# Optimization experiments

Hardware: AMD Instinct MI355X
Metric: run time of the kernel (lower is better)

Reference implementation:

```python
import jax, jax.numpy as jnp
import numpy as np

jax.config.update("jax_enable_x64", True)  # I-BERT's FixedPointMul runs in double precision

# I-BERT IntSoftmax constants
COEF0 = 0.35815147
COEF1 = 0.96963238 / COEF0
COEF2 = 1.0 / COEF0
X0 = -0.6931          # -ln(2)
N_EXP = 30            # large integer n in int_exp
MAX_BIT = 32
OUTPUT_BIT = 8
ACT_BIT = 16

B, H, S = 1, 12, 2048


def sg(x):
    return jax.lax.stop_gradient(x)


def ste_round(x):
    # straight-through round (matches torch round_ste / SymmetricQuantFunction backward)
    return x + sg(jnp.round(x) - x)


def ste_floor(x):
    return x + sg(jnp.floor(x) - x)


def sym_scale(x_min, x_max, bits):
    # symmetric_linear_quantization_params: scale = clamp(max(|min|,|max|),1e-8)/(2^(b-1)-1)
    n = 2 ** (bits - 1) - 1
    s = jnp.maximum(jnp.abs(x_min), jnp.abs(x_max))
    return sg(jnp.maximum(s, 1e-8) / n)


def fixedpoint_mul(pre_act, pre_sf, z_sf, bits):
    # I-BERT fixedpoint_mul: requantize pre_act (granularity pre_sf) to scale z_sf
    # using a 31-bit mantissa frexp decomposition, computed in float64.
    n = 2 ** (bits - 1) - 1
    z_int = ste_round(pre_act.astype(jnp.float64) / pre_sf.astype(jnp.float64))
    new_scale = sg((pre_sf / z_sf).astype(jnp.float64))
    e = jnp.floor(jnp.log2(jnp.abs(new_scale))) + 1.0   # frexp exponent
    m_int = jnp.round((new_scale / 2.0 ** e) * 2.0 ** 31)  # 31-bit mantissa
    out = ste_round(z_int * m_int / 2.0 ** (31.0 - e))
    return jnp.clip(out, -n - 1, n).astype(jnp.float32)


def quant_softmax(x):
    n16 = 2 ** (ACT_BIT - 1) - 1
    # ---- outer QuantAct(16, symmetric), specified min/max = data min/max ----
    sf = sym_scale(sg(x.min()), sg(x.max()), ACT_BIT)
    x_int = jnp.clip(ste_round(x / sf), -n16 - 1, n16)
    quant_x = x_int * sf  # dequantized activation returned by QuantAct
    # ---- IntSoftmax ----
    xi = quant_x / sf
    xi = xi - xi.max(axis=-1, keepdims=True)
    # int_exp: shift-based exponential, exp(x) = 2^(-q) * exp(r), r in (-ln2, 0]
    x0_int = sg(jnp.floor(X0 / sf))               # negative integer
    xi = jnp.maximum(xi, N_EXP * x0_int)
    q = ste_floor(xi / x0_int)
    r = xi - x0_int * q
    # int_polynomial: 2nd-order poly approximation of exp on (-ln2, 0]
    b_int = sg(jnp.floor(COEF1 / sf))
    c_int = sg(jnp.floor(COEF2 / sf ** 2))
    z = r * (r + b_int) + c_int
    exp_sf = sg(COEF0 * sf ** 2) / 2.0 ** N_EXP
    exp_int = jnp.maximum(ste_floor(z * 2.0 ** (N_EXP - q)), 0.0)
    # ---- inner QuantAct(16): requantize exp to 16 bits to avoid overflow ----
    act_sf = sym_scale(sg(exp_int.min()), sg(exp_int.max()), ACT_BIT)
    exp_int16 = fixedpoint_mul(exp_int, exp_sf, act_sf, ACT_BIT)
    # ---- integer normalization to output_bit fixed point ----
    s = exp_int16.sum(axis=-1, keepdims=True)
    factor = ste_floor(2.0 ** MAX_BIT / s)
    out_int = ste_floor(exp_int16 * factor / 2.0 ** (MAX_BIT - OUTPUT_BIT))
    out_sf = 1.0 / 2.0 ** OUTPUT_BIT
    return out_int * out_sf  # softmax probs quantized to 1/256 grid


def setup_inputs() -> dict:
    key = jax.random.key(0)
    x = jax.random.normal(key, (B, H, S, S), dtype=jnp.float32)
    return {"x": x}


def reference(x):
    return quant_softmax(x)
```

## Files before the change

### kernel.cpp

```cpp
#include <hip/hip_runtime.h>
#include <math.h>


#define ROW_S 2048
#define RPB 8
#define P1_BLOCKS (24576 / RPB)

typedef float floatx4 __attribute__((ext_vector_type(4)));

struct Scalars {
    double exp_sf_d;
    double inv_exp_sf;
    double m_int;
    double inv_pow;
    float  sf;
    float  inv_sf;
    float  x0_int;
    float  inv_x0;
    float  b_int;
    float  c_int;
    float  thirty_x0;
    float  _pad;
};

__device__ __forceinline__ float div_rn(float a, float b, float inv) {
    const float q0 = __fmul_rn(a, inv);
    const float r  = __fmaf_rn(-b, q0, a);
    return __fmaf_rn(r, inv, q0);
}
__device__ __forceinline__ double ddiv_rn(double a, double b, double inv) {
    const double q0 = __dmul_rn(a, inv);
    const double r  = __fma_rn(-b, q0, a);
    return __fma_rn(r, inv, q0);
}

__global__ __launch_bounds__(256) void k_rowmax(const float* __restrict__ x,
                                                float* __restrict__ pabs,
                                                float* __restrict__ rowmax) {
    const int t   = threadIdx.x;
    const int rib = t >> 5;
    const int lir = t & 31;
    const size_t base4 = ((size_t)blockIdx.x * RPB + rib) * (ROW_S / 4) + lir;
    const float4* x4 = (const float4*)x;

    float vmax = -INFINITY, amax = 0.0f;
#pragma unroll
    for (int k = 0; k < 16; ++k) {
        float4 v = x4[base4 + (size_t)k * 32];
        vmax = fmaxf(vmax, fmaxf(fmaxf(v.x, v.y), fmaxf(v.z, v.w)));
        amax = fmaxf(amax, fmaxf(fmaxf(fabsf(v.x), fabsf(v.y)),
                                 fmaxf(fabsf(v.z), fabsf(v.w))));
    }
#pragma unroll
    for (int m = 16; m > 0; m >>= 1) vmax = fmaxf(vmax, __shfl_xor(vmax, m));
    if (lir == 0) rowmax[blockIdx.x * RPB + rib] = vmax;
#pragma unroll
    for (int m = 32; m > 0; m >>= 1) amax = fmaxf(amax, __shfl_xor(amax, m));
    __shared__ float sa[4];
    if ((t & 63) == 0) sa[t >> 6] = amax;
    __syncthreads();
    if (t == 0) pabs[blockIdx.x] = fmaxf(fmaxf(sa[0], sa[1]), fmaxf(sa[2], sa[3]));
}

__global__ __launch_bounds__(256) void k_scalars(const float* __restrict__ pabs,
                                                 Scalars* __restrict__ sc) {
    const int tid = threadIdx.x;
    float amax = 0.0f;
    for (int i = tid; i < P1_BLOCKS; i += 256) amax = fmaxf(amax, pabs[i]);
#pragma unroll
    for (int m = 32; m > 0; m >>= 1) amax = fmaxf(amax, __shfl_xor(amax, m));
    __shared__ float sa[4];
    const int wave = tid >> 6, lane = tid & 63;
    if (lane == 0) sa[wave] = amax;
    __syncthreads();
    if (tid == 0) {
        const float sabs = fmaxf(fmaxf(sa[0], sa[1]), fmaxf(sa[2], sa[3]));
        const float sf    = __fdiv_rn(fmaxf(sabs, 1e-8f), 32767.0f);
        const float x0i   = floorf(__fdiv_rn((float)(-0.6931), sf));
        const float sfsq  = __fmul_rn(sf, sf);
        const float b_int = floorf(__fdiv_rn((float)(0.96963238 / 0.35815147), sf));
        const float c_int = floorf(__fdiv_rn((float)(1.0 / 0.35815147), sfsq));
        const float exp_sf = __fdiv_rn(__fmul_rn((float)(0.35815147), sfsq), 1073741824.0f);
        const float emax   = __fmul_rn(c_int, 1073741824.0f);
        const float act_sf = __fdiv_rn(fmaxf(emax, 1e-8f), 32767.0f);
        const float  nsf = __fdiv_rn(exp_sf, act_sf);
        const double ns  = (double)nsf;
        int E;
        (void)frexp(ns, &E);
        const double m_int = rint(ldexp(ns, 31 - E));
        sc->exp_sf_d   = (double)exp_sf;
        sc->inv_exp_sf = 1.0 / (double)exp_sf;
        sc->m_int      = m_int;
        sc->inv_pow    = ldexp(1.0, E - 31);
        sc->sf         = sf;
        sc->inv_sf     = __fdiv_rn(1.0f, sf);
        sc->x0_int     = x0i;
        sc->inv_x0     = __fdiv_rn(1.0f, x0i);
        sc->b_int      = b_int;
        sc->c_int      = c_int;
        sc->thirty_x0  = __fmul_rn(30.0f, x0i);
    }
}

__global__ __launch_bounds__(256) void k_row(const float* __restrict__ x,
                                             float* __restrict__ out,
                                             const Scalars* __restrict__ scp,
                                             const float* __restrict__ rowmax) {
    const int tid = threadIdx.x;
    const size_t rowbase = (size_t)blockIdx.x * ROW_S;
    const float4* x4 = (const float4*)(x + rowbase);
    floatx4* o4 = (floatx4*)(out + rowbase);

    const float4 va = x4[tid];
    const float4 vb = x4[tid + 256];
    const float  rm = rowmax[blockIdx.x];

    const Scalars sc = *scp;
    const float sf = sc.sf, inv_sf = sc.inv_sf;

    float ximax;
    {
        float t = rintf(div_rn(rm, sf, inv_sf));
        t = fminf(fmaxf(t, -32768.0f), 32767.0f);
        t = __fmul_rn(t, sf);
        ximax = div_rn(t, sf, inv_sf);
    }

    float xv[8] = {va.x, va.y, va.z, va.w, vb.x, vb.y, vb.z, vb.w};

    float e16[8];
    float ssum = 0.0f;
#pragma unroll
    for (int j = 0; j < 8; ++j) {
        float t = rintf(div_rn(xv[j], sf, inv_sf));
        t = fminf(fmaxf(t, -32768.0f), 32767.0f);
        t = __fmul_rn(t, sf);
        t = div_rn(t, sf, inv_sf);
        const float xs = __fsub_rn(t, ximax);
        const float xm = fmaxf(xs, sc.thirty_x0);
        const float qf = floorf(div_rn(xm, sc.x0_int, sc.inv_x0));
        const float r  = __fsub_rn(xm, __fmul_rn(sc.x0_int, qf));
        const float z  = __fadd_rn(__fmul_rn(r, __fadd_rn(r, sc.b_int)), sc.c_int);
        const int   qi = (int)qf;
        const float p2 = __int_as_float((157 - qi) << 23);
        const float ei = fmaxf(floorf(__fmul_rn(z, p2)), 0.0f);
        const double a  = (double)ei;
        const double zi = rint(ddiv_rn(a, sc.exp_sf_d, sc.inv_exp_sf));
        double ov = rint(__dmul_rn(__dmul_rn(zi, sc.m_int), sc.inv_pow));
        ov = fmin(fmax(ov, -32768.0), 32767.0);
        const float v = (float)ov;
        e16[j] = v;
        ssum += v;
    }

    __shared__ float red[4];
    const int wave = tid >> 6, lane = tid & 63;
#pragma unroll
    for (int m = 32; m > 0; m >>= 1) ssum += __shfl_xor(ssum, m);
    if (lane == 0) red[wave] = ssum;
    __syncthreads();
    const float s = ((red[0] + red[1]) + (red[2] + red[3]));
    const float factor = floorf(__fdiv_rn(4294967296.0f, s));

    float ov[8];
#pragma unroll
    for (int j = 0; j < 8; ++j) {
        const float oi = floorf(__fmul_rn(__fmul_rn(e16[j], factor), 5.9604644775390625e-8f));
        ov[j] = __fmul_rn(oi, 0.00390625f);
    }
    floatx4 w0 = {ov[0], ov[1], ov[2], ov[3]};
    floatx4 w1 = {ov[4], ov[5], ov[6], ov[7]};
    __builtin_nontemporal_store(w0, &o4[tid]);
    __builtin_nontemporal_store(w1, &o4[tid + 256]);
}

extern "C" void kernel_launch(void* const* d_in, const int* in_sizes, int n_in,
                              void* d_out, int out_size, void* d_ws, size_t ws_size,
                              hipStream_t stream) {
    const float* x = (const float*)d_in[0];
    float* out = (float*)d_out;
    const int n = in_sizes[0];
    const int rows = n / ROW_S;

    Scalars* sc   = (Scalars*)d_ws;
    float* pabs   = (float*)((char*)d_ws + 256);
    float* rowmax = (float*)((char*)d_ws + 32768);

    k_rowmax<<<P1_BLOCKS, 256, 0, stream>>>(x, pabs, rowmax);
    k_scalars<<<1, 256, 0, stream>>>(pabs, sc);
    k_row<<<rows, 256, 0, stream>>>(x, out, sc, rowmax);
}
```

Baseline: 360.7 us.

## Fuse three kernels into one persistent kernel with a grid-wide barrier

The three launches (row max, scalar computation, row softmax) become a single persistent kernel of 512 blocks. Each block handles 48 rows and meets the others at a global atomic barrier: block 0 computes the shared scalars and releases a flag. The second pass walks the rows in reverse so the most recently read data is likely still in cache (L2/MALL), cutting DRAM re-reads of the input and removing launch gaps. The cost is a spin-wait barrier that can deadlock unless all 512 blocks are co-resident. It also adds a memset of the sync counters, and row max and absolute max now use min/max tracking.

```diff
diff --git a/kernel.cpp b/kernel.cpp
--- a/kernel.cpp
+++ b/kernel.cpp
@@ -3,24 +3,21 @@
 
 
 #define ROW_S 2048
-#define RPB 8
-#define P1_BLOCKS (24576 / RPB)
+#define GRID  512
+#define TPB   256
 
 typedef float floatx4 __attribute__((ext_vector_type(4)));
 
-struct Scalars {
+struct Gsync {
+    unsigned count;
+    unsigned flag;
+    unsigned amax_bits;
+    unsigned _pad;
     double exp_sf_d;
     double inv_exp_sf;
     double m_int;
     double inv_pow;
-    float  sf;
-    float  inv_sf;
-    float  x0_int;
-    float  inv_x0;
-    float  b_int;
-    float  c_int;
-    float  thirty_x0;
-    float  _pad;
+    float  sf, inv_sf, x0_int, inv_x0, b_int, c_int, thirty_x0, _pad2;
 };
 
 __device__ __forceinline__ float div_rn(float a, float b, float inv) {
@@ -34,144 +31,148 @@
     return __fma_rn(r, inv, q0);
 }
 
-__global__ __launch_bounds__(256) void k_rowmax(const float* __restrict__ x,
-                                                float* __restrict__ pabs,
-                                                float* __restrict__ rowmax) {
-    const int t   = threadIdx.x;
-    const int rib = t >> 5;
-    const int lir = t & 31;
-    const size_t base4 = ((size_t)blockIdx.x * RPB + rib) * (ROW_S / 4) + lir;
+__global__ __launch_bounds__(TPB, 2) void k_fused(const float* __restrict__ x,
+                                                  float* __restrict__ out,
+                                                  Gsync* __restrict__ g,
+                                                  int rows) {
+    const int tid  = threadIdx.x;
+    const int wave = tid >> 6, lane = tid & 63;
+    const int rpb   = rows / GRID;
+    const int iters = rpb >> 2;
+    const int row0  = blockIdx.x * rpb;
+
+    __shared__ float rowmax_s[64];
+    __shared__ float amax_s[4];
+
     const float4* x4 = (const float4*)x;
 
-    float vmax = -INFINITY, amax = 0.0f;
+    float vminall = INFINITY, rmall = -INFINITY;
+    for (int k = 0; k < iters; ++k) {
+        const int rl = (k << 2) + wave;
+        const size_t b4 = (size_t)(row0 + rl) * (ROW_S / 4) + lane;
+        float4 v[8];
 #pragma unroll
-    for (int k = 0; k < 16; ++k) {
-        float4 v = x4[base4 + (size_t)k * 32];
-        vmax = fmaxf(vmax, fmaxf(fmaxf(v.x, v.y), fmaxf(v.z, v.w)));
-        amax = fmaxf(amax, fmaxf(fmaxf(fabsf(v.x), fabsf(v.y)),
-                                 fmaxf(fabsf(v.z), fabsf(v.w))));
+        for (int j = 0; j < 8; ++j) v[j] = x4[b4 + 64 * j];
+        float vmax = -INFINITY;
+#pragma unroll
+        for (int j = 0; j < 8; ++j) {
+            vmax    = fmaxf(vmax,    fmaxf(fmaxf(v[j].x, v[j].y), fmaxf(v[j].z, v[j].w)));
+            vminall = fminf(vminall, fminf(fminf(v[j].x, v[j].y), fminf(v[j].z, v[j].w)));
+        }
+#pragma unroll
+        for (int m = 32; m > 0; m >>= 1) vmax = fmaxf(vmax, __shfl_xor(vmax, m));
+        if (lane == 0) rowmax_s[rl] = vmax;
+        rmall = fmaxf(rmall, vmax);
     }
 #pragma unroll
-    for (int m = 16; m > 0; m >>= 1) vmax = fmaxf(vmax, __shfl_xor(vmax, m));
-    if (lir == 0) rowmax[blockIdx.x * RPB + rib] = vmax;
+    for (int m = 32; m > 0; m >>= 1) vminall = fminf(vminall, __shfl_xor(vminall, m));
+    const float am = fmaxf(-vminall, rmall);
+    if (lane == 0) amax_s[wave] = am;
+    __syncthreads();
+
+    if (tid == 0) {
+        const float amax = fmaxf(fmaxf(amax_s[0], amax_s[1]), fmaxf(amax_s[2], amax_s[3]));
+        atomicMax(&g->amax_bits, __float_as_uint(amax));
+        __threadfence();
+        atomicAdd(&g->count, 1u);
+        if (blockIdx.x == 0) {
+            while (__hip_atomic_load(&g->count, __ATOMIC_ACQUIRE, __HIP_MEMORY_SCOPE_AGENT) < GRID) {}
+            const float sabs = __uint_as_float(
+                __hip_atomic_load(&g->amax_bits, __ATOMIC_ACQUIRE, __HIP_MEMORY_SCOPE_AGENT));
+            const float sf    = __fdiv_rn(fmaxf(sabs, 1e-8f), 32767.0f);
+            const float x0i   = floorf(__fdiv_rn((float)(-0.6931), sf));
+            const float sfsq  = __fmul_rn(sf, sf);
+            const float b_int = floorf(__fdiv_rn((float)(0.96963238 / 0.35815147), sf));
+            const float c_int = floorf(__fdiv_rn((float)(1.0 / 0.35815147), sfsq));
+            const float exp_sf = __fdiv_rn(__fmul_rn((float)(0.35815147), sfsq), 1073741824.0f);
+            const float emax   = __fmul_rn(c_int, 1073741824.0f);
+            const float act_sf = __fdiv_rn(fmaxf(emax, 1e-8f), 32767.0f);
+            const float  nsf = __fdiv_rn(exp_sf, act_sf);
+            const double ns  = (double)nsf;
+            int E;
+            (void)frexp(ns, &E);
+            g->exp_sf_d   = (double)exp_sf;
+            g->inv_exp_sf = 1.0 / (double)exp_sf;
+            g->m_int      = rint(ldexp(ns, 31 - E));
+            g->inv_pow    = ldexp(1.0, E - 31);
+            g->sf         = sf;
+            g->inv_sf     = __fdiv_rn(1.0f, sf);
+            g->x0_int     = x0i;
+            g->inv_x0     = __fdiv_rn(1.0f, x0i);
+            g->b_int      = b_int;
+            g->c_int      = c_int;
+            g->thirty_x0  = __fmul_rn(30.0f, x0i);
+            __threadfence();
+            __hip_atomic_store(&g->flag, 1u, __ATOMIC_RELEASE, __HIP_MEMORY_SCOPE_AGENT);
+        }
+    }
+    while (__hip_atomic_load(&g->flag, __ATOMIC_ACQUIRE, __HIP_MEMORY_SCOPE_AGENT) == 0u) {}
+    __syncthreads();
+
+    const float  sf     = g->sf,      inv_sf = g->inv_sf;
+    const float  x0i    = g->x0_int,  inv_x0 = g->inv_x0;
+    const float  b_int  = g->b_int,   c_int  = g->c_int, t30 = g->thirty_x0;
+    const double esf    = g->exp_sf_d, iesf  = g->inv_exp_sf;
+    const double mi     = g->m_int,    ipow  = g->inv_pow;
+    (void)c_int;
+
+    floatx4* o4 = (floatx4*)out;
+    for (int k = iters - 1; k >= 0; --k) {
+        const int rl = (k << 2) + wave;
+        const size_t b4 = (size_t)(row0 + rl) * (ROW_S / 4) + lane;
+        const float rm = rowmax_s[rl];
+        float ximax;
+        {
+            float t = rintf(div_rn(rm, sf, inv_sf));
+            t = fminf(fmaxf(t, -32768.0f), 32767.0f);
+            t = __fmul_rn(t, sf);
+            ximax = div_rn(t, sf, inv_sf);
+        }
+        float4 v[8];
 #pragma unroll
-    for (int m = 32; m > 0; m >>= 1) amax = fmaxf(amax, __shfl_xor(amax, m));
-    __shared__ float sa[4];
-    if ((t & 63) == 0) sa[t >> 6] = amax;
-    __syncthreads();
-    if (t == 0) pabs[blockIdx.x] = fmaxf(fmaxf(sa[0], sa[1]), fmaxf(sa[2], sa[3]));
-}
-
-__global__ __launch_bounds__(256) void k_scalars(const float* __restrict__ pabs,
-                                                 Scalars* __restrict__ sc) {
-    const int tid = threadIdx.x;
-    float amax = 0.0f;
-    for (int i = tid; i < P1_BLOCKS; i += 256) amax = fmaxf(amax, pabs[i]);
+        for (int j = 0; j < 8; ++j) v[j] = x4[b4 + 64 * j];
+        float e16[32];
+        float ssum = 0.0f;
 #pragma unroll
-    for (int m = 32; m > 0; m >>= 1) amax = fmaxf(amax, __shfl_xor(amax, m));
-    __shared__ float sa[4];
-    const int wave = tid >> 6, lane = tid & 63;
-    if (lane == 0) sa[wave] = amax;
-    __syncthreads();
-    if (tid == 0) {
-        const float sabs = fmaxf(fmaxf(sa[0], sa[1]), fmaxf(sa[2], sa[3]));
-        const float sf    = __fdiv_rn(fmaxf(sabs, 1e-8f), 32767.0f);
-        const float x0i   = floorf(__fdiv_rn((float)(-0.6931), sf));
-        const float sfsq  = __fmul_rn(sf, sf);
-        const float b_int = floorf(__fdiv_rn((float)(0.96963238 / 0.35815147), sf));
-        const float c_int = floorf(__fdiv_rn((float)(1.0 / 0.35815147), sfsq));
-        const float exp_sf = __fdiv_rn(__fmul_rn((float)(0.35815147), sfsq), 1073741824.0f);
-        const float emax   = __fmul_rn(c_int, 1073741824.0f);
-        const float act_sf = __fdiv_rn(fmaxf(emax, 1e-8f), 32767.0f);
-        const float  nsf = __fdiv_rn(exp_sf, act_sf);
-        const double ns  = (double)nsf;
-        int E;
-        (void)frexp(ns, &E);
-        const double m_int = rint(ldexp(ns, 31 - E));
-        sc->exp_sf_d   = (double)exp_sf;
-        sc->inv_exp_sf = 1.0 / (double)exp_sf;
-        sc->m_int      = m_int;
-        sc->inv_pow    = ldexp(1.0, E - 31);
-        sc->sf         = sf;
-        sc->inv_sf     = __fdiv_rn(1.0f, sf);
-        sc->x0_int     = x0i;
-        sc->inv_x0     = __fdiv_rn(1.0f, x0i);
-        sc->b_int      = b_int;
-        sc->c_int      = c_int;
-        sc->thirty_x0  = __fmul_rn(30.0f, x0i);
+        for (int j = 0; j < 8; ++j) {
+            const float xv[4] = {v[j].x, v[j].y, v[j].z, v[j].w};
+#pragma unroll
+            for (int c = 0; c < 4; ++c) {
+                float t = rintf(div_rn(xv[c], sf, inv_sf));
+                t = fminf(fmaxf(t, -32768.0f), 32767.0f);
+                t = __fmul_rn(t, sf);
+                t = div_rn(t, sf, inv_sf);
+                const float xs = __fsub_rn(t, ximax);
+                const float xm = fmaxf(xs, t30);
+                const float qf = floorf(div_rn(xm, x0i, inv_x0));
+                const float r  = __fsub_rn(xm, __fmul_rn(x0i, qf));
+                const float z  = __fadd_rn(__fmul_rn(r, __fadd_rn(r, b_int)), c_int);
+                const int   qi = (int)qf;
+                const float p2 = __int_as_float((157 - qi) << 23);
+                const float ei = fmaxf(floorf(__fmul_rn(z, p2)), 0.0f);
+                const double zi = rint(ddiv_rn((double)ei, esf, iesf));
+                double ov = rint(__dmul_rn(__dmul_rn(zi, mi), ipow));
+                ov = fmin(fmax(ov, -32768.0), 32767.0);
+                const float w = (float)ov;
+                e16[4 * j + c] = w;
+                ssum += w;
+            }
+        }
+#pragma unroll
+        for (int m = 32; m > 0; m >>= 1) ssum += __shfl_xor(ssum, m);
+        const float factor = floorf(__fdiv_rn(4294967296.0f, ssum));
+#pragma unroll
+        for (int j = 0; j < 8; ++j) {
+            floatx4 w;
+#pragma unroll
+            for (int c = 0; c < 4; ++c) {
+                const float oi = floorf(__fmul_rn(__fmul_rn(e16[4 * j + c], factor),
+                                                  5.9604644775390625e-8f));
+                w[c] = __fmul_rn(oi, 0.00390625f);
+            }
+            __builtin_nontemporal_store(w, &o4[b4 + 64 * j]);
+        }
     }
-}
-
-__global__ __launch_bounds__(256) void k_row(const float* __restrict__ x,
-                                             float* __restrict__ out,
-                                             const Scalars* __restrict__ scp,
-                                             const float* __restrict__ rowmax) {
-    const int tid = threadIdx.x;
-    const size_t rowbase = (size_t)blockIdx.x * ROW_S;
-    const float4* x4 = (const float4*)(x + rowbase);
-    floatx4* o4 = (floatx4*)(out + rowbase);
-
-    const float4 va = x4[tid];
-    const float4 vb = x4[tid + 256];
-    const float  rm = rowmax[blockIdx.x];
-
-    const Scalars sc = *scp;
-    const float sf = sc.sf, inv_sf = sc.inv_sf;
-
-    float ximax;
-    {
-        float t = rintf(div_rn(rm, sf, inv_sf));
-        t = fminf(fmaxf(t, -32768.0f), 32767.0f);
-        t = __fmul_rn(t, sf);
-        ximax = div_rn(t, sf, inv_sf);
-    }
-
-    float xv[8] = {va.x, va.y, va.z, va.w, vb.x, vb.y, vb.z, vb.w};
-
-    float e16[8];
-    float ssum = 0.0f;
-#pragma unroll
-    for (int j = 0; j < 8; ++j) {
-        float t = rintf(div_rn(xv[j], sf, inv_sf));
-        t = fminf(fmaxf(t, -32768.0f), 32767.0f);
-        t = __fmul_rn(t, sf);
-        t = div_rn(t, sf, inv_sf);
-        const float xs = __fsub_rn(t, ximax);
-        const float xm = fmaxf(xs, sc.thirty_x0);
-        const float qf = floorf(div_rn(xm, sc.x0_int, sc.inv_x0));
-        const float r  = __fsub_rn(xm, __fmul_rn(sc.x0_int, qf));
-        const float z  = __fadd_rn(__fmul_rn(r, __fadd_rn(r, sc.b_int)), sc.c_int);
-        const int   qi = (int)qf;
-        const float p2 = __int_as_float((157 - qi) << 23);
-        const float ei = fmaxf(floorf(__fmul_rn(z, p2)), 0.0f);
-        const double a  = (double)ei;
-        const double zi = rint(ddiv_rn(a, sc.exp_sf_d, sc.inv_exp_sf));
-        double ov = rint(__dmul_rn(__dmul_rn(zi, sc.m_int), sc.inv_pow));
-        ov = fmin(fmax(ov, -32768.0), 32767.0);
-        const float v = (float)ov;
-        e16[j] = v;
-        ssum += v;
-    }
-
-    __shared__ float red[4];
-    const int wave = tid >> 6, lane = tid & 63;
-#pragma unroll
-    for (int m = 32; m > 0; m >>= 1) ssum += __shfl_xor(ssum, m);
-    if (lane == 0) red[wave] = ssum;
-    __syncthreads();
-    const float s = ((red[0] + red[1]) + (red[2] + red[3]));
-    const float factor = floorf(__fdiv_rn(4294967296.0f, s));
-
-    float ov[8];
-#pragma unroll
-    for (int j = 0; j < 8; ++j) {
-        const float oi = floorf(__fmul_rn(__fmul_rn(e16[j], factor), 5.9604644775390625e-8f));
-        ov[j] = __fmul_rn(oi, 0.00390625f);
-    }
-    floatx4 w0 = {ov[0], ov[1], ov[2], ov[3]};
-    floatx4 w1 = {ov[4], ov[5], ov[6], ov[7]};
-    __builtin_nontemporal_store(w0, &o4[tid]);
-    __builtin_nontemporal_store(w1, &o4[tid + 256]);
 }
 
 extern "C" void kernel_launch(void* const* d_in, const int* in_sizes, int n_in,
@@ -182,11 +183,7 @@
     const int n = in_sizes[0];
     const int rows = n / ROW_S;
 
-    Scalars* sc   = (Scalars*)d_ws;
-    float* pabs   = (float*)((char*)d_ws + 256);
-    float* rowmax = (float*)((char*)d_ws + 32768);
-
-    k_rowmax<<<P1_BLOCKS, 256, 0, stream>>>(x, pabs, rowmax);
-    k_scalars<<<1, 256, 0, stream>>>(pabs, sc);
-    k_row<<<rows, 256, 0, stream>>>(x, out, sc, rowmax);
+    Gsync* g = (Gsync*)d_ws;
+    hipMemsetAsync(d_ws, 0, 64, stream);
+    k_fused<<<GRID, TPB, 0, stream>>>(x, out, g, rows);
 }
```

After: 538.3 us. 1.49x slower.

## Replace scalar-reduction kernel with atomicMax and recompute scalars per block

Applied to the files above, without the earlier changes.

The single-block scalar kernel is removed. Each pass-1 block now folds its absolute max into a global word with an integer atomicMax on the float bits, which is valid because the values are non-negative. Every row block then recomputes the quantization scalars from that global max. This trades one kernel launch and a serial tiny kernel for a memset, contended atomics, and redundant per-block scalar math including divisions and frexp/ldexp.

```diff
diff --git a/kernel.cpp b/kernel.cpp
--- a/kernel.cpp
+++ b/kernel.cpp
@@ -7,21 +7,6 @@
 #define P1_BLOCKS (24576 / RPB)
 
 typedef float floatx4 __attribute__((ext_vector_type(4)));
-
-struct Scalars {
-    double exp_sf_d;
-    double inv_exp_sf;
-    double m_int;
-    double inv_pow;
-    float  sf;
-    float  inv_sf;
-    float  x0_int;
-    float  inv_x0;
-    float  b_int;
-    float  c_int;
-    float  thirty_x0;
-    float  _pad;
-};
 
 __device__ __forceinline__ float div_rn(float a, float b, float inv) {
     const float q0 = __fmul_rn(a, inv);
@@ -34,9 +19,9 @@
     return __fma_rn(r, inv, q0);
 }
 
-__global__ __launch_bounds__(256) void k_rowmax(const float* __restrict__ x,
-                                                float* __restrict__ pabs,
-                                                float* __restrict__ rowmax) {
+__global__ __launch_bounds__(256) void k_pass1(const float* __restrict__ x,
+                                               unsigned* __restrict__ amax_bits,
+                                               float* __restrict__ rowmax) {
     const int t   = threadIdx.x;
     const int rib = t >> 5;
     const int lir = t & 31;
@@ -59,52 +44,15 @@
     __shared__ float sa[4];
     if ((t & 63) == 0) sa[t >> 6] = amax;
     __syncthreads();
-    if (t == 0) pabs[blockIdx.x] = fmaxf(fmaxf(sa[0], sa[1]), fmaxf(sa[2], sa[3]));
-}
-
-__global__ __launch_bounds__(256) void k_scalars(const float* __restrict__ pabs,
-                                                 Scalars* __restrict__ sc) {
-    const int tid = threadIdx.x;
-    float amax = 0.0f;
-    for (int i = tid; i < P1_BLOCKS; i += 256) amax = fmaxf(amax, pabs[i]);
-#pragma unroll
-    for (int m = 32; m > 0; m >>= 1) amax = fmaxf(amax, __shfl_xor(amax, m));
-    __shared__ float sa[4];
-    const int wave = tid >> 6, lane = tid & 63;
-    if (lane == 0) sa[wave] = amax;
-    __syncthreads();
-    if (tid == 0) {
-        const float sabs = fmaxf(fmaxf(sa[0], sa[1]), fmaxf(sa[2], sa[3]));
-        const float sf    = __fdiv_rn(fmaxf(sabs, 1e-8f), 32767.0f);
-        const float x0i   = floorf(__fdiv_rn((float)(-0.6931), sf));
-        const float sfsq  = __fmul_rn(sf, sf);
-        const float b_int = floorf(__fdiv_rn((float)(0.96963238 / 0.35815147), sf));
-        const float c_int = floorf(__fdiv_rn((float)(1.0 / 0.35815147), sfsq));
-        const float exp_sf = __fdiv_rn(__fmul_rn((float)(0.35815147), sfsq), 1073741824.0f);
-        const float emax   = __fmul_rn(c_int, 1073741824.0f);
-        const float act_sf = __fdiv_rn(fmaxf(emax, 1e-8f), 32767.0f);
-        const float  nsf = __fdiv_rn(exp_sf, act_sf);
-        const double ns  = (double)nsf;
-        int E;
-        (void)frexp(ns, &E);
-        const double m_int = rint(ldexp(ns, 31 - E));
-        sc->exp_sf_d   = (double)exp_sf;
-        sc->inv_exp_sf = 1.0 / (double)exp_sf;
-        sc->m_int      = m_int;
-        sc->inv_pow    = ldexp(1.0, E - 31);
-        sc->sf         = sf;
-        sc->inv_sf     = __fdiv_rn(1.0f, sf);
-        sc->x0_int     = x0i;
-        sc->inv_x0     = __fdiv_rn(1.0f, x0i);
-        sc->b_int      = b_int;
-        sc->c_int      = c_int;
-        sc->thirty_x0  = __fmul_rn(30.0f, x0i);
+    if (t == 0) {
+        const float bm = fmaxf(fmaxf(sa[0], sa[1]), fmaxf(sa[2], sa[3]));
+        atomicMax(amax_bits, __float_as_uint(bm));
     }
 }
 
 __global__ __launch_bounds__(256) void k_row(const float* __restrict__ x,
                                              float* __restrict__ out,
-                                             const Scalars* __restrict__ scp,
+                                             const unsigned* __restrict__ amax_bits,
                                              const float* __restrict__ rowmax) {
     const int tid = threadIdx.x;
     const size_t rowbase = (size_t)blockIdx.x * ROW_S;
@@ -114,9 +62,27 @@
     const float4 va = x4[tid];
     const float4 vb = x4[tid + 256];
     const float  rm = rowmax[blockIdx.x];
+    const float  sabs = __uint_as_float(*amax_bits);
 
-    const Scalars sc = *scp;
-    const float sf = sc.sf, inv_sf = sc.inv_sf;
+    const float sf     = __fdiv_rn(fmaxf(sabs, 1e-8f), 32767.0f);
+    const float inv_sf = __fdiv_rn(1.0f, sf);
+    const float x0i    = floorf(__fdiv_rn((float)(-0.6931), sf));
+    const float inv_x0 = __fdiv_rn(1.0f, x0i);
+    const float sfsq   = __fmul_rn(sf, sf);
+    const float b_int  = floorf(__fdiv_rn((float)(0.96963238 / 0.35815147), sf));
+    const float c_int  = floorf(__fdiv_rn((float)(1.0 / 0.35815147), sfsq));
+    const float exp_sf = __fdiv_rn(__fmul_rn((float)(0.35815147), sfsq), 1073741824.0f);
+    const float t30    = __fmul_rn(30.0f, x0i);
+    const float emax   = __fmul_rn(c_int, 1073741824.0f);
+    const float act_sf = __fdiv_rn(fmaxf(emax, 1e-8f), 32767.0f);
+    const float  nsf = __fdiv_rn(exp_sf, act_sf);
+    const double ns  = (double)nsf;
+    int E;
+    (void)frexp(ns, &E);
+    const double mi   = rint(ldexp(ns, 31 - E));
+    const double ipow = ldexp(1.0, E - 31);
+    const double esf  = (double)exp_sf;
+    const double iesf = 1.0 / esf;
 
     float ximax;
     {
@@ -137,16 +103,15 @@
         t = __fmul_rn(t, sf);
         t = div_rn(t, sf, inv_sf);
         const float xs = __fsub_rn(t, ximax);
-        const float xm = fmaxf(xs, sc.thirty_x0);
-        const float qf = floorf(div_rn(xm, sc.x0_int, sc.inv_x0));
-        const float r  = __fsub_rn(xm, __fmul_rn(sc.x0_int, qf));
-        const float z  = __fadd_rn(__fmul_rn(r, __fadd_rn(r, sc.b_int)), sc.c_int);
+        const float xm = fmaxf(xs, t30);
+        const float qf = floorf(div_rn(xm, x0i, inv_x0));
+        const float r  = __fsub_rn(xm, __fmul_rn(x0i, qf));
+        const float z  = __fadd_rn(__fmul_rn(r, __fadd_rn(r, b_int)), c_int);
         const int   qi = (int)qf;
         const float p2 = __int_as_float((157 - qi) << 23);
         const float ei = fmaxf(floorf(__fmul_rn(z, p2)), 0.0f);
-        const double a  = (double)ei;
-        const double zi = rint(ddiv_rn(a, sc.exp_sf_d, sc.inv_exp_sf));
-        double ov = rint(__dmul_rn(__dmul_rn(zi, sc.m_int), sc.inv_pow));
+        const double zi = rint(ddiv_rn((double)ei, esf, iesf));
+        double ov = rint(__dmul_rn(__dmul_rn(zi, mi), ipow));
         ov = fmin(fmax(ov, -32768.0), 32767.0);
         const float v = (float)ov;
         e16[j] = v;
@@ -182,11 +147,10 @@
     const int n = in_sizes[0];
     const int rows = n / ROW_S;
 
-    Scalars* sc   = (Scalars*)d_ws;
-    float* pabs   = (float*)((char*)d_ws + 256);
-    float* rowmax = (float*)((char*)d_ws + 32768);
+    unsigned* amax_bits = (unsigned*)d_ws;
+    float* rowmax = (float*)((char*)d_ws + 256);
 
-    k_rowmax<<<P1_BLOCKS, 256, 0, stream>>>(x, pabs, rowmax);
-    k_scalars<<<1, 256, 0, stream>>>(pabs, sc);
-    k_row<<<rows, 256, 0, stream>>>(x, out, sc, rowmax);
+    hipMemsetAsync(d_ws, 0, 64, stream);
+    k_pass1<<<P1_BLOCKS, 256, 0, stream>>>(x, amax_bits, rowmax);
+    k_row<<<rows, 256, 0, stream>>>(x, out, amax_bits, rowmax);
 }
```

Measured after the change: 381.8 us. 5.9% more time.
